# Kernel optimization log

Hardware: AMD Instinct MI355X
Metric: run time of the kernel (lower is better)

## Reference

```python
import jax, jax.numpy as jnp
import numpy as np

N = 100_000      # total nodes in batched graph
NE = 800_000     # total edges
G = 1_000        # number of graphs in batch
V_DIM = 128      # node feat dim (== H_DIM, required by GRUCell usage)
E_DIM = 64       # edge feat dim
H_DIM = 128      # hidden dim
K_HEAD = 4       # multi-scale interaction heads


def _leaky(x):
    return jnp.where(x >= 0, x, 0.1 * x)


def _gru_cell(x, h, Wih, Whh, bih, bhh):
    # torch nn.GRUCell math; Wih/Whh stored as [in, 3*h] with (r,z,n) chunk order
    gi = x @ Wih + bih
    gh = h @ Whh + bhh
    ir, iz, inn = jnp.split(gi, 3, axis=-1)
    hr, hz, hn = jnp.split(gh, 3, axis=-1)
    r = jax.nn.sigmoid(ir + hr)
    z = jax.nn.sigmoid(iz + hz)
    n = jnp.tanh(inn + r * hn)
    return (1.0 - z) * n + z * h


def setup_inputs() -> dict:
    key = jax.random.key(0)
    ks = iter(jax.random.split(key, 48))
    def rn(shape, scale=0.05):
        return (jax.random.normal(next(ks), shape) * scale).astype(jnp.float32)
    inp = {}
    inp["v"] = rn((N, V_DIM), 1.0)
    inp["e"] = rn((NE, E_DIM), 1.0)
    inp["s"] = rn((G, V_DIM), 1.0)
    inp["edge_src"] = jax.random.randint(next(ks), (NE,), 0, N)
    inp["edge_dst"] = jax.random.randint(next(ks), (NE,), 0, N)
    inp["node_graph"] = jnp.repeat(jnp.arange(G), N // G)  # sorted segment ids
    # top-level linears (stored [in, out])
    inp["A_w"] = rn((V_DIM, H_DIM)); inp["A_b"] = rn((H_DIM,))
    inp["mA_w"] = rn((K_HEAD, V_DIM, H_DIM)); inp["mA_b"] = rn((K_HEAD, H_DIM))
    inp["mB_w"] = rn((K_HEAD, V_DIM, H_DIM)); inp["mB_b"] = rn((K_HEAD, H_DIM))
    inp["mC_w"] = rn((K_HEAD, H_DIM)); inp["mC_b"] = rn((K_HEAD,))
    inp["mD_w"] = rn((K_HEAD, V_DIM, H_DIM)); inp["mD_b"] = rn((K_HEAD, H_DIM))
    inp["B_w"] = rn((H_DIM * K_HEAD, H_DIM)); inp["B_b"] = rn((H_DIM,))
    inp["C_w"] = rn((V_DIM, H_DIM)); inp["C_b"] = rn((H_DIM,))
    inp["K_w"] = rn((E_DIM, H_DIM)); inp["K_b"] = rn((H_DIM,))
    inp["E_w"] = rn((H_DIM + V_DIM, H_DIM)); inp["E_b"] = rn((H_DIM,))
    for pfx in ("gm", "gs"):
        inp[pfx + "_A_w"] = rn((H_DIM, H_DIM)); inp[pfx + "_A_b"] = rn((H_DIM,))
        inp[pfx + "_B_w"] = rn((H_DIM, H_DIM)); inp[pfx + "_B_b"] = rn((H_DIM,))
        inp[pfx + "_Wih"] = rn((H_DIM, 3 * H_DIM)); inp[pfx + "_Whh"] = rn((H_DIM, 3 * H_DIM))
        inp[pfx + "_bih"] = rn((3 * H_DIM,)); inp[pfx + "_bhh"] = rn((3 * H_DIM,))
    return inp


def reference(v, e, s, edge_src, edge_dst, node_graph,
              A_w, A_b, mA_w, mA_b, mB_w, mB_b, mC_w, mC_b, mD_w, mD_b,
              B_w, B_b, C_w, C_b, K_w, K_b, E_w, E_b,
              gm_A_w, gm_A_b, gm_B_w, gm_B_b, gm_Wih, gm_Whh, gm_bih, gm_bhh,
              gs_A_w, gs_A_b, gs_B_w, gs_B_b, gs_Wih, gs_Whh, gs_bih, gs_bhh):
    # super -> super
    s2s = jnp.tanh(s @ A_w + A_b)                                       # [G,H]
    # multi-head node->super attention pooling (Multi_scale_interaction)
    d_node = jnp.tanh(jnp.einsum('nv,kvh->knh', v, mA_w) + mA_b[:, None, :])     # [K,N,H]
    d_super = jnp.tanh(jnp.einsum('gv,kvh->kgh', s, mB_w) + mB_b[:, None, :])    # [K,G,H]
    a = jnp.einsum('knh,kh->nk', d_node * d_super[:, node_graph, :], mC_w) + mC_b[None, :]  # [N,K]
    a_max = jax.ops.segment_max(a, node_graph, num_segments=G, indices_are_sorted=True)
    a_exp = jnp.exp(a - a_max[node_graph])
    denom = jax.ops.segment_sum(a_exp, node_graph, num_segments=G, indices_are_sorted=True)
    attn = a_exp / denom[node_graph]                                    # per-graph softmax, [N,K]
    d_v = jnp.einsum('nv,kvh->nkh', v, mD_w) + mD_b[None, :, :]         # [N,K,H]
    pooled = jax.ops.segment_sum(d_v * attn[:, :, None], node_graph, num_segments=G,
                                 indices_are_sorted=True)               # [G,K,H]
    m2s = jnp.tanh(pooled.reshape(G, K_HEAD * H_DIM) @ B_w + B_b)       # [G,H]
    # super -> node broadcast
    s2m = jnp.tanh(s @ C_w + C_b)[node_graph]                           # [N,H]
    # edge-wise message: leaky_relu(K(e) * v_src) summed into destination node
    ve = _leaky((e @ K_w + K_b) * v[edge_src])                          # [E,H]
    sve = jax.ops.segment_sum(ve, edge_dst, num_segments=N)             # [N,H]
    m2m = _leaky(jnp.concatenate([sve, v], axis=1) @ E_w + E_b)         # [N,H]
    # adaptive GRU gate: node update
    z_m = jax.nn.sigmoid(m2m @ gm_A_w + gm_A_b + s2m @ gm_B_w + gm_B_b)
    h_m = z_m * s2m + (1.0 - z_m) * m2m
    update_v = _gru_cell(v, h_m, gm_Wih, gm_Whh, gm_bih, gm_bhh)
    # adaptive GRU gate: supernode update
    z_s = jax.nn.sigmoid(s2s @ gs_A_w + gs_A_b + m2s @ gs_B_w + gs_B_b)
    h_s = z_s * m2s + (1.0 - z_s) * s2s
    update_s = _gru_cell(s, h_s, gs_Wih, gs_Whh, gs_bih, gs_bhh)
    return (update_v, update_s)
```

## Files before the change

kernel.cpp:

```cpp
#include <hip/hip_runtime.h>

#define NN   100000
#define NEDG 800000
#define NG   1000
#define HD   128
#define EDIM 64

#define NB3 (NEDG / 64)
#define NB2 ((NN + 63) / 64)
#define NB6 ((NN + 63) / 64)
#define NB4 (NN / 32)

typedef unsigned short u16;
typedef __bf16 bf16x8 __attribute__((ext_vector_type(8)));
typedef float f32x4 __attribute__((ext_vector_type(4)));
typedef u16 u16x8 __attribute__((ext_vector_type(8)));
typedef unsigned u32x4 __attribute__((ext_vector_type(4)));

#define MFMA16(a, b, c) __builtin_amdgcn_mfma_f32_16x16x32_bf16(a, b, c, 0, 0, 0)

#define WS_E    0
#define WS_GA   4096
#define WS_WIH  6144
#define WS_WHH  12288
#define WS_MA0  18432
#define WS_KW   26624
#define WS_LANES 27648

#define BF(base, NTT, ks, nt, lane) \
    (*(const bf16x8*)(wsw + (size_t)((base) + (((ks) * (NTT) + (nt)) * 64 + (lane))) * 8))

__device__ __forceinline__ float sigmoidf_(float x) { return 1.0f / (1.0f + __expf(-x)); }
__device__ __forceinline__ float tanhf_(float x) {
    float ax = fabsf(x);
    float e  = __expf(-2.0f * ax);
    float t  = (1.0f - e) / (1.0f + e);
    return copysignf(t, x);
}
__device__ __forceinline__ float leaky_(float x) { return x >= 0.f ? x : 0.1f * x; }
__device__ __forceinline__ u16 f2bf(float x) {
    union { float f; unsigned u; } c; c.f = x;
    unsigned r = c.u + 0x7FFF + ((c.u >> 16) & 1);
    return (u16)(r >> 16);
}
__device__ __forceinline__ float bfbits2f(unsigned hw) {
    union { unsigned u; float f; } c; c.u = hw << 16; return c.f;
}
__device__ __forceinline__ unsigned pack2bf(float lo, float hi) {
    return (unsigned)f2bf(lo) | ((unsigned)f2bf(hi) << 16);
}
__device__ __forceinline__ bf16x8 mk8(const float* __restrict__ p) {
    float4 a = *(const float4*)p;
    float4 b = *(const float4*)(p + 4);
    union { u32x4 u; bf16x8 v; } c;
    c.u[0] = pack2bf(a.x, a.y);
    c.u[1] = pack2bf(a.z, a.w);
    c.u[2] = pack2bf(b.x, b.y);
    c.u[3] = pack2bf(b.z, b.w);
    return c.v;
}

__device__ __forceinline__ void stg4(u16* lds, int P, int r, int c0, float4 v4) {
    int byteoff = (c0 << 1) ^ ((r & 7) << 4);
    u16* p = lds + r * P + (byteoff >> 1);
    p[0] = f2bf(v4.x); p[1] = f2bf(v4.y); p[2] = f2bf(v4.z); p[3] = f2bf(v4.w);
}
__device__ __forceinline__ void stg1(u16* lds, int P, int r, int c, u16 val) {
    int byteoff = (c << 1) ^ ((r & 7) << 4);
    lds[r * P + (byteoff >> 1)] = val;
}
__device__ __forceinline__ bf16x8 ldA(const u16* lds, int P, int r, int ks, int hi) {
    int byteoff = (ks * 64 + (hi << 4)) ^ ((r & 7) << 4);
    return *(const bf16x8*)(lds + r * P + (byteoff >> 1));
}

__global__ __launch_bounds__(256) void wconv(
    const float* __restrict__ E_w, const float* __restrict__ gmA_w,
    const float* __restrict__ Wih, const float* __restrict__ Whh,
    const float* __restrict__ mA_w, const float* __restrict__ K_w,
    u16* __restrict__ dst)
{
    int t = blockIdx.x * 256 + threadIdx.x;
    if (t >= WS_LANES) return;
    const float* W; int N; int local;
    if (t < 4096)       { W = E_w;  N = 128; local = t; }
    else if (t < 6144)  { W = gmA_w; N = 128; local = t - 4096; }
    else if (t < 12288) { W = Wih;  N = 384; local = t - 6144; }
    else if (t < 18432) { W = Whh;  N = 384; local = t - 12288; }
    else if (t < 26624) { int k = (t - 18432) >> 11; W = mA_w + k * 128 * 128; N = 128; local = (t - 18432) & 2047; }
    else                { W = K_w;  N = 128; local = t - 26624; }
    int lane = local & 63;
    int fid  = local >> 6;
    int NT = N >> 4;
    int ks = fid / NT, nt = fid - ks * NT;
    int krow = ks * 32 + ((lane >> 4) << 3);
    int col  = nt * 16 + (lane & 15);
    u16* d = dst + (size_t)t * 8;
    #pragma unroll
    for (int j = 0; j < 8; j++) d[j] = f2bf(W[(size_t)(krow + j) * N + col]);
}

__global__ __launch_bounds__(256) void k_hist(const int* __restrict__ edst, int* __restrict__ cnt) {
    int i = blockIdx.x * 256 + threadIdx.x;
    if (i < NEDG) atomicAdd(&cnt[edst[i]], 1);
}

__global__ __launch_bounds__(256) void k_scan1(const int* __restrict__ cnt,
                                               int* __restrict__ excl, int* __restrict__ bsum) {
    __shared__ int sd[256];
    int t = threadIdx.x, b = blockIdx.x;
    int base = b * 1024 + t * 4;
    int v0 = (base + 0 < NN) ? cnt[base + 0] : 0;
    int v1 = (base + 1 < NN) ? cnt[base + 1] : 0;
    int v2 = (base + 2 < NN) ? cnt[base + 2] : 0;
    int v3 = (base + 3 < NN) ? cnt[base + 3] : 0;
    int s = v0 + v1 + v2 + v3;
    sd[t] = s;
    __syncthreads();
    for (int off = 1; off < 256; off <<= 1) {
        int x = (t >= off) ? sd[t - off] : 0;
        __syncthreads();
        sd[t] += x;
        __syncthreads();
    }
    int incl = sd[t];
    int ex = incl - s;
    if (base + 0 < NN) excl[base + 0] = ex;
    if (base + 1 < NN) excl[base + 1] = ex + v0;
    if (base + 2 < NN) excl[base + 2] = ex + v0 + v1;
    if (base + 3 < NN) excl[base + 3] = ex + v0 + v1 + v2;
    if (t == 255) bsum[b] = incl;
}

#define NSCB 98
__global__ void k_scan2(int* __restrict__ bsum) {
    if (threadIdx.x == 0 && blockIdx.x == 0) {
        int run = 0;
        for (int i = 0; i < NSCB; i++) { int t = bsum[i]; bsum[i] = run; run += t; }
    }
}

__global__ __launch_bounds__(256) void k_scan3(const int* __restrict__ excl,
                                               const int* __restrict__ bsum,
                                               int* __restrict__ start) {
    int i = blockIdx.x * 256 + threadIdx.x;
    if (i < NN) start[i] = excl[i] + bsum[i >> 10];
}

__global__ __launch_bounds__(256) void k_scatter(const int* __restrict__ edst,
                                                 int* __restrict__ start,
                                                 int* __restrict__ perm) {
    int i = blockIdx.x * 256 + threadIdx.x;
    if (i < NEDG) {
        int pos = atomicAdd(&start[edst[i]], 1);
        perm[pos] = i;
    }
}

__global__ __launch_bounds__(128) void k1_graph(
    const float* __restrict__ s,
    const float* __restrict__ A_w, const float* __restrict__ A_b,
    const float* __restrict__ mB_w, const float* __restrict__ mB_b,
    const float* __restrict__ mC_w,
    const float* __restrict__ C_w, const float* __restrict__ C_b,
    const float* __restrict__ gmB_w, const float* __restrict__ gmA_b, const float* __restrict__ gmB_b,
    float* __restrict__ s2s, float* __restrict__ wkg,
    float* __restrict__ s2m_tab, float* __restrict__ t2)
{
    __shared__ float sm[HD];
    __shared__ float sm2[HD];
    const int g = blockIdx.x, t = threadIdx.x;
    sm[t] = s[g * HD + t];
    __syncthreads();
    {
        float a = 0.f;
        #pragma unroll 8
        for (int i = 0; i < HD; i++) a = fmaf(sm[i], A_w[i * HD + t], a);
        s2s[g * HD + t] = tanhf_(a + A_b[t]);
    }
    for (int k = 0; k < 4; k++) {
        float a = 0.f;
        const float* W = mB_w + k * HD * HD;
        #pragma unroll 8
        for (int i = 0; i < HD; i++) a = fmaf(sm[i], W[i * HD + t], a);
        float d = tanhf_(a + mB_b[k * HD + t]);
        wkg[(k * NG + g) * HD + t] = d * mC_w[k * HD + t];
    }
    float s2m;
    {
        float a = 0.f;
        #pragma unroll 8
        for (int i = 0; i < HD; i++) a = fmaf(sm[i], C_w[i * HD + t], a);
        s2m = tanhf_(a + C_b[t]);
        s2m_tab[g * HD + t] = s2m;
    }
    sm2[t] = s2m;
    __syncthreads();
    {
        float a = 0.f;
        #pragma unroll 8
        for (int i = 0; i < HD; i++) a = fmaf(sm2[i], gmB_w[i * HD + t], a);
        t2[g * HD + t] = a + gmA_b[t] + gmB_b[t];
    }
}

__global__ __launch_bounds__(256) void k2_standalone(
    const float* __restrict__ v, const int* __restrict__ ngr,
    const u16* __restrict__ wsw,
    const float* __restrict__ mA_b, const float* __restrict__ mC_b,
    const float* __restrict__ wkg,
    float* __restrict__ aexp, float* __restrict__ denom)
{
    const int tid = threadIdx.x;
    const int lane = tid & 63, w = tid >> 6;
    const int l15 = lane & 15, hi = lane >> 4;
    const int n0 = blockIdx.x * 64 + w * 16;
    const int arow = min(n0 + l15, NN - 1);
    bf16x8 av[4];
    #pragma unroll
    for (int ks = 0; ks < 4; ks++)
        av[ks] = mk8(v + (size_t)arow * HD + ks * 32 + hi * 8);
    int gq[4], nodeq[4];
    #pragma unroll
    for (int q = 0; q < 4; q++) {
        int nd = n0 + hi * 4 + q;
        nodeq[q] = nd;
        gq[q] = ngr[min(nd, NN - 1)];
    }
    for (int k = 0; k < 4; k++) {
        float rs[4] = {0.f, 0.f, 0.f, 0.f};
        const float* bias = mA_b + k * HD;
        #pragma unroll
        for (int nt = 0; nt < 8; nt++) {
            f32x4 acc = {0.f, 0.f, 0.f, 0.f};
            #pragma unroll
            for (int ks = 0; ks < 4; ks++)
                acc = MFMA16(av[ks], BF(WS_MA0 + k * 2048, 8, ks, nt, lane), acc);
            int col = nt * 16 + l15;
            float bb = bias[col];
            #pragma unroll
            for (int q = 0; q < 4; q++)
                rs[q] += tanhf_(acc[q] + bb) * wkg[((size_t)k * NG + gq[q]) * HD + col];
        }
        #pragma unroll
        for (int q = 0; q < 4; q++) {
            float x = rs[q];
            x += __shfl_xor(x, 1); x += __shfl_xor(x, 2);
            x += __shfl_xor(x, 4); x += __shfl_xor(x, 8);
            if (l15 == 0 && nodeq[q] < NN) {
                float ev = __expf(x + mC_b[k]);
                aexp[(size_t)nodeq[q] * 4 + k] = ev;
                atomicAdd(&denom[gq[q] * 4 + k], ev);
            }
        }
    }
}

#define OPW 66
__global__ __launch_bounds__(256) void k3_merge(
    const float* __restrict__ e, const float* __restrict__ v,
    const int* __restrict__ esrc, const int* __restrict__ edst,
    const int* __restrict__ perm,
    const u16* __restrict__ wsw, const float* __restrict__ K_b,
    float* __restrict__ sve)
{
    __shared__ unsigned OUTP[64 * OPW];
    __shared__ int pid[64];
    __shared__ int dsta[64];
    const int tid = threadIdx.x;
    const int e0 = blockIdx.x * 64;
    if (tid < 64) {
        int p = perm[e0 + tid];
        pid[tid] = p;
        dsta[tid] = edst[p];
    }
    const int lane = tid & 63, w = tid >> 6;
    const int l15 = lane & 15, hi = lane >> 4;
    const int rbase = w * 16;
    const int myrow = perm[e0 + rbase + l15];
    bf16x8 ae[2];
    #pragma unroll
    for (int ks = 0; ks < 2; ks++)
        ae[ks] = mk8(e + (size_t)myrow * EDIM + ks * 32 + hi * 8);
    __syncthreads();
    int sq[4];
    #pragma unroll
    for (int q = 0; q < 4; q++) sq[q] = esrc[pid[rbase + hi * 4 + q]];
    u16* OU = (u16*)OUTP;
    #pragma unroll
    for (int nt = 0; nt < 8; nt++) {
        f32x4 acc = {0.f, 0.f, 0.f, 0.f};
        acc = MFMA16(ae[0], BF(WS_KW, 8, 0, nt, lane), acc);
        acc = MFMA16(ae[1], BF(WS_KW, 8, 1, nt, lane), acc);
        int col = nt * 16 + l15;
        float kb = K_b[col];
        #pragma unroll
        for (int q = 0; q < 4; q++) {
            float val = leaky_((acc[q] + kb) * v[(size_t)sq[q] * HD + col]);
            OU[(rbase + hi * 4 + q) * (OPW * 2) + col] = f2bf(val);
        }
    }
    __syncthreads();
    {
        const int cp = tid & 63;
        const int qr = tid >> 6;
        const int r0 = qr * 16;
        int dcur = dsta[r0];
        unsigned x = OUTP[r0 * OPW + cp];
        float a0 = bfbits2f(x & 0xffff), a1 = bfbits2f(x >> 16);
        #pragma unroll
        for (int i = 1; i < 16; i++) {
            int r = r0 + i;
            int d = dsta[r];
            unsigned y = OUTP[r * OPW + cp];
            float y0 = bfbits2f(y & 0xffff), y1 = bfbits2f(y >> 16);
            if (d == dcur) { a0 += y0; a1 += y1; }
            else {
                atomicAdd(&sve[(size_t)dcur * HD + cp * 2 + 0], a0);
                atomicAdd(&sve[(size_t)dcur * HD + cp * 2 + 1], a1);
                dcur = d; a0 = y0; a1 = y1;
            }
        }
        atomicAdd(&sve[(size_t)dcur * HD + cp * 2 + 0], a0);
        atomicAdd(&sve[(size_t)dcur * HD + cp * 2 + 1], a1);
    }
}

__global__ __launch_bounds__(256) void k3_edge_unsorted(
    const float* __restrict__ e, const float* __restrict__ v,
    const int* __restrict__ esrc, const int* __restrict__ edst,
    const u16* __restrict__ wsw, const float* __restrict__ K_b,
    float* __restrict__ sve)
{
    const int tid = threadIdx.x;
    const int e0 = blockIdx.x * 64;
    const int lane = tid & 63, w = tid >> 6;
    const int l15 = lane & 15, hi = lane >> 4;
    const int rbase = w * 16;
    const int myrow = e0 + rbase + l15;
    bf16x8 ae[2];
    #pragma unroll
    for (int ks = 0; ks < 2; ks++)
        ae[ks] = mk8(e + (size_t)myrow * EDIM + ks * 32 + hi * 8);
    int sq[4], dq[4];
    #pragma unroll
    for (int q = 0; q < 4; q++) {
        int ei = e0 + rbase + hi * 4 + q;
        sq[q] = esrc[ei]; dq[q] = edst[ei];
    }
    #pragma unroll
    for (int nt = 0; nt < 8; nt++) {
        f32x4 acc = {0.f, 0.f, 0.f, 0.f};
        acc = MFMA16(ae[0], BF(WS_KW, 8, 0, nt, lane), acc);
        acc = MFMA16(ae[1], BF(WS_KW, 8, 1, nt, lane), acc);
        int col = nt * 16 + l15;
        float kb = K_b[col];
        #pragma unroll
        for (int q = 0; q < 4; q++) {
            float val = leaky_((acc[q] + kb) * v[(size_t)sq[q] * HD + col]);
            atomicAdd(&sve[(size_t)dq[q] * HD + col], val);
        }
    }
}

__device__ __forceinline__ void k4_body(
    int bid, int tid,
    const float* __restrict__ v, const int* __restrict__ ngr,
    const float* __restrict__ aexp, const float* __restrict__ denom,
    float* __restrict__ vbar)
{
    const int d = tid & 127;
    const int hf = tid >> 7;
    const int n0 = bid * 32 + hf * 16;
    int gcur = -1;
    float a0 = 0.f, a1 = 0.f, a2 = 0.f, a3 = 0.f;
    float4 rd = make_float4(0.f, 0.f, 0.f, 0.f);
    for (int nd = 0; nd < 16; nd++) {
        int n = n0 + nd;
        int g = ngr[n];
        if (g != gcur) {
            if (gcur >= 0) {
                atomicAdd(&vbar[(gcur * 4 + 0) * HD + d], a0);
                atomicAdd(&vbar[(gcur * 4 + 1) * HD + d], a1);
                atomicAdd(&vbar[(gcur * 4 + 2) * HD + d], a2);
                atomicAdd(&vbar[(gcur * 4 + 3) * HD + d], a3);
                a0 = a1 = a2 = a3 = 0.f;
            }
            float4 dn = *(const float4*)&denom[g * 4];
            rd = make_float4(1.f / dn.x, 1.f / dn.y, 1.f / dn.z, 1.f / dn.w);
            gcur = g;
        }
        float4 ae = *(const float4*)&aexp[n * 4];
        float vv = v[(size_t)n * HD + d];
        a0 = fmaf(ae.x * rd.x, vv, a0);
        a1 = fmaf(ae.y * rd.y, vv, a1);
        a2 = fmaf(ae.z * rd.z, vv, a2);
        a3 = fmaf(ae.w * rd.w, vv, a3);
    }
    atomicAdd(&vbar[(gcur * 4 + 0) * HD + d], a0);
    atomicAdd(&vbar[(gcur * 4 + 1) * HD + d], a1);
    atomicAdd(&vbar[(gcur * 4 + 2) * HD + d], a2);
    atomicAdd(&vbar[(gcur * 4 + 3) * HD + d], a3);
}

__device__ __forceinline__ void k6_body(
    int bid, int tid, u16* T,
    const float* __restrict__ v, const int* __restrict__ ngr,
    const float* __restrict__ sve, const u16* __restrict__ wsw,
    const float* __restrict__ E_b,
    const float* __restrict__ s2m_tab, const float* __restrict__ t2,
    const float* __restrict__ bih, const float* __restrict__ bhh,
    float* __restrict__ out_v)
{
    const int lane = tid & 63;
    const int l15 = lane & 15, hi = lane >> 4;
    const int n0 = bid * 64 + (tid >> 6) * 16;
    const int arow = min(n0 + l15, NN - 1);
    bf16x8 av[4], ax[4];
    #pragma unroll
    for (int ks = 0; ks < 4; ks++) {
        av[ks] = mk8(v   + (size_t)arow * HD + ks * 32 + hi * 8);
        ax[ks] = mk8(sve + (size_t)arow * HD + ks * 32 + hi * 8);
    }
    int gq[4], nodeq[4];
    #pragma unroll
    for (int q = 0; q < 4; q++) {
        int nd = n0 + hi * 4 + q;
        nodeq[q] = nd;
        gq[q] = ngr[min(nd, NN - 1)];
    }
    unsigned m2mp[8][2];
    #pragma unroll
    for (int nt = 0; nt < 8; nt++) {
        f32x4 acc = {0.f, 0.f, 0.f, 0.f};
        #pragma unroll
        for (int ks = 0; ks < 4; ks++) acc = MFMA16(ax[ks], BF(WS_E, 8, ks, nt, lane), acc);
        #pragma unroll
        for (int ks = 0; ks < 4; ks++) acc = MFMA16(av[ks], BF(WS_E, 8, 4 + ks, nt, lane), acc);
        float eb = E_b[nt * 16 + l15];
        float m0 = leaky_(acc[0] + eb), m1 = leaky_(acc[1] + eb);
        float m2 = leaky_(acc[2] + eb), m3 = leaky_(acc[3] + eb);
        m2mp[nt][0] = pack2bf(m0, m1);
        m2mp[nt][1] = pack2bf(m2, m3);
        int col = nt * 16 + l15;
        stg1(T, 128, hi * 4 + 0, col, (u16)(m2mp[nt][0] & 0xffff));
        stg1(T, 128, hi * 4 + 1, col, (u16)(m2mp[nt][0] >> 16));
        stg1(T, 128, hi * 4 + 2, col, (u16)(m2mp[nt][1] & 0xffff));
        stg1(T, 128, hi * 4 + 3, col, (u16)(m2mp[nt][1] >> 16));
    }
    bf16x8 am[4];
    #pragma unroll
    for (int ks = 0; ks < 4; ks++) am[ks] = ldA(T, 128, l15, ks, hi);
    unsigned hmp[8][2];
    #pragma unroll
    for (int nt = 0; nt < 8; nt++) {
        f32x4 acc = {0.f, 0.f, 0.f, 0.f};
        #pragma unroll
        for (int ks = 0; ks < 4; ks++) acc = MFMA16(am[ks], BF(WS_GA, 8, ks, nt, lane), acc);
        int col = nt * 16 + l15;
        float m2mq[4] = { bfbits2f(m2mp[nt][0] & 0xffff), bfbits2f(m2mp[nt][0] >> 16),
                          bfbits2f(m2mp[nt][1] & 0xffff), bfbits2f(m2mp[nt][1] >> 16) };
        float hm[4];
        #pragma unroll
        for (int q = 0; q < 4; q++) {
            int g = gq[q];
            float z = sigmoidf_(acc[q] + t2[(size_t)g * HD + col]);
            hm[q] = z * s2m_tab[(size_t)g * HD + col] + (1.f - z) * m2mq[q];
        }
        hmp[nt][0] = pack2bf(hm[0], hm[1]);
        hmp[nt][1] = pack2bf(hm[2], hm[3]);
        stg1(T, 128, hi * 4 + 0, col, (u16)(hmp[nt][0] & 0xffff));
        stg1(T, 128, hi * 4 + 1, col, (u16)(hmp[nt][0] >> 16));
        stg1(T, 128, hi * 4 + 2, col, (u16)(hmp[nt][1] & 0xffff));
        stg1(T, 128, hi * 4 + 3, col, (u16)(hmp[nt][1] >> 16));
    }
    bf16x8 ah[4];
    #pragma unroll
    for (int ks = 0; ks < 4; ks++) ah[ks] = ldA(T, 128, l15, ks, hi);
    #pragma unroll
    for (int nt = 0; nt < 8; nt++) {
        f32x4 air = {0.f,0.f,0.f,0.f}, aiz = {0.f,0.f,0.f,0.f}, ain = {0.f,0.f,0.f,0.f};
        f32x4 ahr = {0.f,0.f,0.f,0.f}, ahz = {0.f,0.f,0.f,0.f}, ahn = {0.f,0.f,0.f,0.f};
        #pragma unroll
        for (int ks = 0; ks < 4; ks++) {
            air = MFMA16(av[ks], BF(WS_WIH, 24, ks, nt,      lane), air);
            ahr = MFMA16(ah[ks], BF(WS_WHH, 24, ks, nt,      lane), ahr);
            aiz = MFMA16(av[ks], BF(WS_WIH, 24, ks, nt + 8,  lane), aiz);
            ahz = MFMA16(ah[ks], BF(WS_WHH, 24, ks, nt + 8,  lane), ahz);
            ain = MFMA16(av[ks], BF(WS_WIH, 24, ks, nt + 16, lane), ain);
            ahn = MFMA16(ah[ks], BF(WS_WHH, 24, ks, nt + 16, lane), ahn);
        }
        int col = nt * 16 + l15;
        float br  = bih[col] + bhh[col];
        float bz  = bih[HD + col] + bhh[HD + col];
        float bi3 = bih[2 * HD + col];
        float bh3 = bhh[2 * HD + col];
        float hmq[4] = { bfbits2f(hmp[nt][0] & 0xffff), bfbits2f(hmp[nt][0] >> 16),
                         bfbits2f(hmp[nt][1] & 0xffff), bfbits2f(hmp[nt][1] >> 16) };
        #pragma unroll
        for (int q = 0; q < 4; q++) {
            float r   = sigmoidf_(air[q] + ahr[q] + br);
            float z   = sigmoidf_(aiz[q] + ahz[q] + bz);
            float nnv = tanhf_(ain[q] + bi3 + r * (ahn[q] + bh3));
            if (nodeq[q] < NN)
                out_v[(size_t)nodeq[q] * HD + col] = (1.f - z) * nnv + z * hmq[q];
        }
    }
}

__global__ __launch_bounds__(256) void mega2(
    const float* __restrict__ v, const int* __restrict__ ngr,
    const float* __restrict__ sve, const u16* __restrict__ wsw,
    const float* __restrict__ E_b,
    const float* __restrict__ s2m_tab, const float* __restrict__ t2,
    const float* __restrict__ bih, const float* __restrict__ bhh,
    const float* __restrict__ aexp, const float* __restrict__ denom,
    float* __restrict__ out_v, float* __restrict__ vbar)
{
    __shared__ u16 TT[4][16 * 128];
    const int bid = blockIdx.x, tid = threadIdx.x;
    if (bid < NB6) {
        k6_body(bid, tid, TT[tid >> 6], v, ngr, sve, wsw, E_b, s2m_tab, t2, bih, bhh, out_v);
    } else {
        k4_body(bid - NB6, tid, v, ngr, aexp, denom, vbar);
    }
}

__global__ __launch_bounds__(128) void k5_super(
    const float* __restrict__ s, const float* __restrict__ vbar,
    const float* __restrict__ mD_w, const float* __restrict__ mD_b,
    const float* __restrict__ B_w, const float* __restrict__ B_b,
    const float* __restrict__ s2s,
    const float* __restrict__ gsA_w, const float* __restrict__ gsA_b,
    const float* __restrict__ gsB_w, const float* __restrict__ gsB_b,
    const float* __restrict__ gsWih, const float* __restrict__ gsWhh,
    const float* __restrict__ gsbih, const float* __restrict__ gsbhh,
    float* __restrict__ out_s)
{
    __shared__ float vb[4 * HD];
    __shared__ float p[4 * HD];
    __shared__ float m2s_l[HD];
    __shared__ float s2s_l[HD];
    __shared__ float hs_l[HD];
    __shared__ float srow[HD];
    const int g = blockIdx.x, t = threadIdx.x;
    #pragma unroll
    for (int l = 0; l < 4; l++) vb[t + HD * l] = vbar[(size_t)g * 4 * HD + t + HD * l];
    srow[t]  = s[g * HD + t];
    s2s_l[t] = s2s[g * HD + t];
    __syncthreads();
    for (int k = 0; k < 4; k++) {
        float a = 0.f;
        const float* W = mD_w + k * HD * HD;
        #pragma unroll 8
        for (int i = 0; i < HD; i++) a = fmaf(vb[k * HD + i], W[i * HD + t], a);
        p[k * HD + t] = a + mD_b[k * HD + t];
    }
    __syncthreads();
    float m2s;
    {
        float a = 0.f;
        #pragma unroll 8
        for (int j = 0; j < 4 * HD; j++) a = fmaf(p[j], B_w[j * HD + t], a);
        m2s = tanhf_(a + B_b[t]);
        m2s_l[t] = m2s;
    }
    __syncthreads();
    float hs;
    {
        float za = 0.f, zb = 0.f;
        #pragma unroll 8
        for (int i = 0; i < HD; i++) {
            za = fmaf(s2s_l[i], gsA_w[i * HD + t], za);
            zb = fmaf(m2s_l[i], gsB_w[i * HD + t], zb);
        }
        float z = sigmoidf_(za + gsA_b[t] + zb + gsB_b[t]);
        hs = z * m2s + (1.f - z) * s2s_l[t];
        hs_l[t] = hs;
    }
    __syncthreads();
    float gi0 = 0.f, gh0 = 0.f, gi1 = 0.f, gh1 = 0.f, gi2 = 0.f, gh2 = 0.f;
    #pragma unroll 4
    for (int i = 0; i < HD; i++) {
        float sv = srow[i], hv = hs_l[i];
        gi0 = fmaf(sv, gsWih[i * 384 + t], gi0);
        gh0 = fmaf(hv, gsWhh[i * 384 + t], gh0);
        gi1 = fmaf(sv, gsWih[i * 384 + 128 + t], gi1);
        gh1 = fmaf(hv, gsWhh[i * 384 + 128 + t], gh1);
        gi2 = fmaf(sv, gsWih[i * 384 + 256 + t], gi2);
        gh2 = fmaf(hv, gsWhh[i * 384 + 256 + t], gh2);
    }
    float r  = sigmoidf_(gi0 + gsbih[t] + gh0 + gsbhh[t]);
    float z2 = sigmoidf_(gi1 + gsbih[128 + t] + gh1 + gsbhh[128 + t]);
    float nn = tanhf_(gi2 + gsbih[256 + t] + r * (gh2 + gsbhh[256 + t]));
    out_s[g * HD + t] = (1.f - z2) * nn + z2 * hs;
}

extern "C" void kernel_launch(void* const* d_in, const int* in_sizes, int n_in,
                              void* d_out, int out_size, void* d_ws, size_t ws_size,
                              hipStream_t stream)
{
    const float* v    = (const float*)d_in[0];
    const float* e    = (const float*)d_in[1];
    const float* s    = (const float*)d_in[2];
    const int*   esrc = (const int*)d_in[3];
    const int*   edst = (const int*)d_in[4];
    const int*   ngr  = (const int*)d_in[5];
    const float* A_w  = (const float*)d_in[6];
    const float* A_b  = (const float*)d_in[7];
    const float* mA_w = (const float*)d_in[8];
    const float* mA_b = (const float*)d_in[9];
    const float* mB_w = (const float*)d_in[10];
    const float* mB_b = (const float*)d_in[11];
    const float* mC_w = (const float*)d_in[12];
    const float* mC_b = (const float*)d_in[13];
    const float* mD_w = (const float*)d_in[14];
    const float* mD_b = (const float*)d_in[15];
    const float* B_w  = (const float*)d_in[16];
    const float* B_b  = (const float*)d_in[17];
    const float* C_w  = (const float*)d_in[18];
    const float* C_b  = (const float*)d_in[19];
    const float* K_w  = (const float*)d_in[20];
    const float* K_b  = (const float*)d_in[21];
    const float* E_w  = (const float*)d_in[22];
    const float* E_b  = (const float*)d_in[23];
    const float* gmA_w = (const float*)d_in[24];
    const float* gmA_b = (const float*)d_in[25];
    const float* gmB_w = (const float*)d_in[26];
    const float* gmB_b = (const float*)d_in[27];
    const float* gmWih = (const float*)d_in[28];
    const float* gmWhh = (const float*)d_in[29];
    const float* gmbih = (const float*)d_in[30];
    const float* gmbhh = (const float*)d_in[31];
    const float* gsA_w = (const float*)d_in[32];
    const float* gsA_b = (const float*)d_in[33];
    const float* gsB_w = (const float*)d_in[34];
    const float* gsB_b = (const float*)d_in[35];
    const float* gsWih = (const float*)d_in[36];
    const float* gsWhh = (const float*)d_in[37];
    const float* gsbih = (const float*)d_in[38];
    const float* gsbhh = (const float*)d_in[39];

    float* ws      = (float*)d_ws;
    float* sve     = ws;
    float* aexp    = sve + 12800000;
    float* denom   = aexp + 400000;
    float* wkg     = denom + 4000;
    float* s2s     = wkg + 512000;
    float* s2m_tab = s2s + 128000;
    float* t2      = s2m_tab + 128000;
    float* vbar    = t2 + 128000;
    u16*   wswz    = (u16*)(vbar + 512000);
    int*   isc     = (int*)(wswz + 221184);
    int*   cnt     = isc;
    int*   excl    = cnt + 100000;
    int*   bsum    = excl + 100000;
    int*   startp  = bsum + 128;
    int*   perm    = startp + 100000;
    const size_t NEED_SORT = ((size_t)(perm + 800000 - (int*)d_ws)) * 4;
    const bool do_sort = ws_size >= NEED_SORT;

    hipMemsetAsync(sve, 0, (size_t)12800000 * 4, stream);
    hipMemsetAsync(denom, 0, (size_t)4000 * 4, stream);
    hipMemsetAsync(vbar, 0, (size_t)512000 * 4, stream);

    float* out_v = (float*)d_out;
    float* out_s = out_v + (size_t)NN * HD;

    wconv<<<(WS_LANES + 255) / 256, 256, 0, stream>>>(E_w, gmA_w, gmWih, gmWhh, mA_w, K_w, wswz);
    k1_graph<<<NG, 128, 0, stream>>>(s, A_w, A_b, mB_w, mB_b, mC_w, C_w, C_b,
                                     gmB_w, gmA_b, gmB_b, s2s, wkg, s2m_tab, t2);
    if (do_sort) {
        hipMemsetAsync(cnt, 0, (size_t)100000 * 4, stream);
        k_hist<<<(NEDG + 255) / 256, 256, 0, stream>>>(edst, cnt);
        k_scan1<<<NSCB, 256, 0, stream>>>(cnt, excl, bsum);
        k_scan2<<<1, 64, 0, stream>>>(bsum);
        k_scan3<<<(NN + 255) / 256, 256, 0, stream>>>(excl, bsum, startp);
        k_scatter<<<(NEDG + 255) / 256, 256, 0, stream>>>(edst, startp, perm);
    }
    k2_standalone<<<NB2, 256, 0, stream>>>(v, ngr, wswz, mA_b, mC_b, wkg, aexp, denom);
    if (do_sort) {
        k3_merge<<<NB3, 256, 0, stream>>>(e, v, esrc, edst, perm, wswz, K_b, sve);
    } else {
        k3_edge_unsorted<<<NEDG / 64, 256, 0, stream>>>(e, v, esrc, edst, wswz, K_b, sve);
    }
    mega2<<<NB6 + NB4, 256, 0, stream>>>(v, ngr, sve, wswz, E_b, s2m_tab, t2,
                                         gmbih, gmbhh, aexp, denom, out_v, vbar);
    k5_super<<<NG, 128, 0, stream>>>(s, vbar, mD_w, mD_b, B_w, B_b, s2s,
                                     gsA_w, gsA_b, gsB_w, gsB_b,
                                     gsWih, gsWhh, gsbih, gsbhh, out_s);
}
```

Before: 710.9 us.

## Fuse setup kernels and memsets into combined launches, fold scan3 into scatter

Merges the weight conversion, per-graph kernel and all zero-fills (sve, cnt, vbar, denom) into one block-partitioned launch. It then co-launches the edge histogram with the attention-logit kernel. It also removes the separate start-offset kernel: the scatter now computes `excl+bsum` inline and ranks edges by decrementing the counts. The goal is to cut launch and memset overhead and the serialization gaps between small kernels. In exchange, grids become heterogeneous, and cnt is zeroed and histogrammed even on the unsorted path.

Result: faster. 679.7 us (median of 2 runs) (-4.4%).

```diff
diff --git a/kernel.cpp b/kernel.cpp
--- a/kernel.cpp
+++ b/kernel.cpp
@@ -10,6 +10,12 @@
 #define NB2 ((NN + 63) / 64)
 #define NB6 ((NN + 63) / 64)
 #define NB4 (NN / 32)
+#define W0B 108
+#define MH_HIST 3125
+#define Z_F4 3200000
+#define Z_TOT 3300000
+#define ZB ((Z_TOT + 255) / 256)
+#define M0_GRID (W0B + NG + ZB)
 
 typedef unsigned short u16;
 typedef __bf16 bf16x8 __attribute__((ext_vector_type(8)));
@@ -60,11 +66,6 @@
     return c.v;
 }
 
-__device__ __forceinline__ void stg4(u16* lds, int P, int r, int c0, float4 v4) {
-    int byteoff = (c0 << 1) ^ ((r & 7) << 4);
-    u16* p = lds + r * P + (byteoff >> 1);
-    p[0] = f2bf(v4.x); p[1] = f2bf(v4.y); p[2] = f2bf(v4.z); p[3] = f2bf(v4.w);
-}
 __device__ __forceinline__ void stg1(u16* lds, int P, int r, int c, u16 val) {
     int byteoff = (c << 1) ^ ((r & 7) << 4);
     lds[r * P + (byteoff >> 1)] = val;
@@ -74,14 +75,13 @@
     return *(const bf16x8*)(lds + r * P + (byteoff >> 1));
 }
 
-__global__ __launch_bounds__(256) void wconv(
+__device__ __forceinline__ void wconv_body(
+    int t,
     const float* __restrict__ E_w, const float* __restrict__ gmA_w,
     const float* __restrict__ Wih, const float* __restrict__ Whh,
     const float* __restrict__ mA_w, const float* __restrict__ K_w,
     u16* __restrict__ dst)
 {
-    int t = blockIdx.x * 256 + threadIdx.x;
-    if (t >= WS_LANES) return;
     const float* W; int N; int local;
     if (t < 4096)       { W = E_w;  N = 128; local = t; }
     else if (t < 6144)  { W = gmA_w; N = 128; local = t - 4096; }
@@ -100,9 +100,158 @@
     for (int j = 0; j < 8; j++) d[j] = f2bf(W[(size_t)(krow + j) * N + col]);
 }
 
-__global__ __launch_bounds__(256) void k_hist(const int* __restrict__ edst, int* __restrict__ cnt) {
-    int i = blockIdx.x * 256 + threadIdx.x;
-    if (i < NEDG) atomicAdd(&cnt[edst[i]], 1);
+__device__ __forceinline__ void k1_body(
+    int g, int t,
+    const float* __restrict__ s,
+    const float* __restrict__ A_w, const float* __restrict__ A_b,
+    const float* __restrict__ mB_w, const float* __restrict__ mB_b,
+    const float* __restrict__ mC_w,
+    const float* __restrict__ C_w, const float* __restrict__ C_b,
+    const float* __restrict__ gmB_w, const float* __restrict__ gmA_b, const float* __restrict__ gmB_b,
+    float* __restrict__ s2s, float* __restrict__ wkg,
+    float* __restrict__ s2m_tab, float* __restrict__ t2,
+    float* __restrict__ vbar, float* __restrict__ denom)
+{
+    __shared__ float sm[HD];
+    __shared__ float sm2[HD];
+    if (t < HD) sm[t] = s[g * HD + t];
+    else {
+        int i = t - 128;
+        #pragma unroll
+        for (int j = 0; j < 4; j++) vbar[(size_t)g * 512 + i + 128 * j] = 0.f;
+        if (i < 4) denom[g * 4 + i] = 0.f;
+    }
+    __syncthreads();
+    float s2m = 0.f;
+    if (t < HD) {
+        {
+            float a = 0.f;
+            #pragma unroll 8
+            for (int i = 0; i < HD; i++) a = fmaf(sm[i], A_w[i * HD + t], a);
+            s2s[g * HD + t] = tanhf_(a + A_b[t]);
+        }
+        for (int k = 0; k < 4; k++) {
+            float a = 0.f;
+            const float* W = mB_w + k * HD * HD;
+            #pragma unroll 8
+            for (int i = 0; i < HD; i++) a = fmaf(sm[i], W[i * HD + t], a);
+            float d = tanhf_(a + mB_b[k * HD + t]);
+            wkg[(k * NG + g) * HD + t] = d * mC_w[k * HD + t];
+        }
+        {
+            float a = 0.f;
+            #pragma unroll 8
+            for (int i = 0; i < HD; i++) a = fmaf(sm[i], C_w[i * HD + t], a);
+            s2m = tanhf_(a + C_b[t]);
+            s2m_tab[g * HD + t] = s2m;
+            sm2[t] = s2m;
+        }
+    }
+    __syncthreads();
+    if (t < HD) {
+        float a = 0.f;
+        #pragma unroll 8
+        for (int i = 0; i < HD; i++) a = fmaf(sm2[i], gmB_w[i * HD + t], a);
+        t2[g * HD + t] = a + gmA_b[t] + gmB_b[t];
+    }
+}
+
+__global__ __launch_bounds__(256) void mega0(
+    const float* __restrict__ E_w, const float* __restrict__ gmA_w,
+    const float* __restrict__ Wih, const float* __restrict__ Whh,
+    const float* __restrict__ mA_w, const float* __restrict__ K_w,
+    u16* __restrict__ wswz,
+    const float* __restrict__ s,
+    const float* __restrict__ A_w, const float* __restrict__ A_b,
+    const float* __restrict__ mB_w, const float* __restrict__ mB_b,
+    const float* __restrict__ mC_w,
+    const float* __restrict__ C_w, const float* __restrict__ C_b,
+    const float* __restrict__ gmB_w, const float* __restrict__ gmA_b, const float* __restrict__ gmB_b,
+    float* __restrict__ s2s, float* __restrict__ wkg,
+    float* __restrict__ s2m_tab, float* __restrict__ t2,
+    float* __restrict__ vbar, float* __restrict__ denom,
+    float* __restrict__ sve, int* __restrict__ cnt)
+{
+    const int bid = blockIdx.x, tid = threadIdx.x;
+    if (bid < W0B) {
+        wconv_body(bid * 256 + tid, E_w, gmA_w, Wih, Whh, mA_w, K_w, wswz);
+    } else if (bid < W0B + NG) {
+        k1_body(bid - W0B, tid, s, A_w, A_b, mB_w, mB_b, mC_w, C_w, C_b,
+                gmB_w, gmA_b, gmB_b, s2s, wkg, s2m_tab, t2, vbar, denom);
+    } else {
+        long idx = (long)(bid - W0B - NG) * 256 + tid;
+        if (idx < Z_F4) ((float4*)sve)[idx] = make_float4(0.f, 0.f, 0.f, 0.f);
+        else if (idx < Z_TOT) cnt[idx - Z_F4] = 0;
+    }
+}
+
+__device__ __forceinline__ void k2_body(
+    int bid, int tid,
+    const float* __restrict__ v, const int* __restrict__ ngr,
+    const u16* __restrict__ wsw,
+    const float* __restrict__ mA_b, const float* __restrict__ mC_b,
+    const float* __restrict__ wkg,
+    float* __restrict__ aexp, float* __restrict__ denom)
+{
+    const int lane = tid & 63, w = tid >> 6;
+    const int l15 = lane & 15, hi = lane >> 4;
+    const int n0 = bid * 64 + w * 16;
+    const int arow = min(n0 + l15, NN - 1);
+    bf16x8 av[4];
+    #pragma unroll
+    for (int ks = 0; ks < 4; ks++)
+        av[ks] = mk8(v + (size_t)arow * HD + ks * 32 + hi * 8);
+    int gq[4], nodeq[4];
+    #pragma unroll
+    for (int q = 0; q < 4; q++) {
+        int nd = n0 + hi * 4 + q;
+        nodeq[q] = nd;
+        gq[q] = ngr[min(nd, NN - 1)];
+    }
+    for (int k = 0; k < 4; k++) {
+        float rs[4] = {0.f, 0.f, 0.f, 0.f};
+        const float* bias = mA_b + k * HD;
+        #pragma unroll
+        for (int nt = 0; nt < 8; nt++) {
+            f32x4 acc = {0.f, 0.f, 0.f, 0.f};
+            #pragma unroll
+            for (int ks = 0; ks < 4; ks++)
+                acc = MFMA16(av[ks], BF(WS_MA0 + k * 2048, 8, ks, nt, lane), acc);
+            int col = nt * 16 + l15;
+            float bb = bias[col];
+            #pragma unroll
+            for (int q = 0; q < 4; q++)
+                rs[q] += tanhf_(acc[q] + bb) * wkg[((size_t)k * NG + gq[q]) * HD + col];
+        }
+        #pragma unroll
+        for (int q = 0; q < 4; q++) {
+            float x = rs[q];
+            x += __shfl_xor(x, 1); x += __shfl_xor(x, 2);
+            x += __shfl_xor(x, 4); x += __shfl_xor(x, 8);
+            if (l15 == 0 && nodeq[q] < NN) {
+                float ev = __expf(x + mC_b[k]);
+                aexp[(size_t)nodeq[q] * 4 + k] = ev;
+                atomicAdd(&denom[gq[q] * 4 + k], ev);
+            }
+        }
+    }
+}
+
+__global__ __launch_bounds__(256) void megaH(
+    const int* __restrict__ edst, int* __restrict__ cnt,
+    const float* __restrict__ v, const int* __restrict__ ngr,
+    const u16* __restrict__ wsw,
+    const float* __restrict__ mA_b, const float* __restrict__ mC_b,
+    const float* __restrict__ wkg,
+    float* __restrict__ aexp, float* __restrict__ denom)
+{
+    const int bid = blockIdx.x, tid = threadIdx.x;
+    if (bid < MH_HIST) {
+        int i = bid * 256 + tid;
+        if (i < NEDG) atomicAdd(&cnt[edst[i]], 1);
+    } else {
+        k2_body(bid - MH_HIST, tid, v, ngr, wsw, mA_b, mC_b, wkg, aexp, denom);
+    }
 }
 
 __global__ __launch_bounds__(256) void k_scan1(const int* __restrict__ cnt,
@@ -140,119 +289,16 @@
     }
 }
 
-__global__ __launch_bounds__(256) void k_scan3(const int* __restrict__ excl,
-                                               const int* __restrict__ bsum,
-                                               int* __restrict__ start) {
-    int i = blockIdx.x * 256 + threadIdx.x;
-    if (i < NN) start[i] = excl[i] + bsum[i >> 10];
-}
-
-__global__ __launch_bounds__(256) void k_scatter(const int* __restrict__ edst,
-                                                 int* __restrict__ start,
-                                                 int* __restrict__ perm) {
+__global__ __launch_bounds__(256) void k_scatter_fused(
+    const int* __restrict__ edst,
+    const int* __restrict__ excl, const int* __restrict__ bsum,
+    int* __restrict__ cnt, int* __restrict__ perm)
+{
     int i = blockIdx.x * 256 + threadIdx.x;
     if (i < NEDG) {
-        int pos = atomicAdd(&start[edst[i]], 1);
-        perm[pos] = i;
-    }
-}
-
-__global__ __launch_bounds__(128) void k1_graph(
-    const float* __restrict__ s,
-    const float* __restrict__ A_w, const float* __restrict__ A_b,
-    const float* __restrict__ mB_w, const float* __restrict__ mB_b,
-    const float* __restrict__ mC_w,
-    const float* __restrict__ C_w, const float* __restrict__ C_b,
-    const float* __restrict__ gmB_w, const float* __restrict__ gmA_b, const float* __restrict__ gmB_b,
-    float* __restrict__ s2s, float* __restrict__ wkg,
-    float* __restrict__ s2m_tab, float* __restrict__ t2)
-{
-    __shared__ float sm[HD];
-    __shared__ float sm2[HD];
-    const int g = blockIdx.x, t = threadIdx.x;
-    sm[t] = s[g * HD + t];
-    __syncthreads();
-    {
-        float a = 0.f;
-        #pragma unroll 8
-        for (int i = 0; i < HD; i++) a = fmaf(sm[i], A_w[i * HD + t], a);
-        s2s[g * HD + t] = tanhf_(a + A_b[t]);
-    }
-    for (int k = 0; k < 4; k++) {
-        float a = 0.f;
-        const float* W = mB_w + k * HD * HD;
-        #pragma unroll 8
-        for (int i = 0; i < HD; i++) a = fmaf(sm[i], W[i * HD + t], a);
-        float d = tanhf_(a + mB_b[k * HD + t]);
-        wkg[(k * NG + g) * HD + t] = d * mC_w[k * HD + t];
-    }
-    float s2m;
-    {
-        float a = 0.f;
-        #pragma unroll 8
-        for (int i = 0; i < HD; i++) a = fmaf(sm[i], C_w[i * HD + t], a);
-        s2m = tanhf_(a + C_b[t]);
-        s2m_tab[g * HD + t] = s2m;
-    }
-    sm2[t] = s2m;
-    __syncthreads();
-    {
-        float a = 0.f;
-        #pragma unroll 8
-        for (int i = 0; i < HD; i++) a = fmaf(sm2[i], gmB_w[i * HD + t], a);
-        t2[g * HD + t] = a + gmA_b[t] + gmB_b[t];
-    }
-}
-
-__global__ __launch_bounds__(256) void k2_standalone(
-    const float* __restrict__ v, const int* __restrict__ ngr,
-    const u16* __restrict__ wsw,
-    const float* __restrict__ mA_b, const float* __restrict__ mC_b,
-    const float* __restrict__ wkg,
-    float* __restrict__ aexp, float* __restrict__ denom)
-{
-    const int tid = threadIdx.x;
-    const int lane = tid & 63, w = tid >> 6;
-    const int l15 = lane & 15, hi = lane >> 4;
-    const int n0 = blockIdx.x * 64 + w * 16;
-    const int arow = min(n0 + l15, NN - 1);
-    bf16x8 av[4];
-    #pragma unroll
-    for (int ks = 0; ks < 4; ks++)
-        av[ks] = mk8(v + (size_t)arow * HD + ks * 32 + hi * 8);
-    int gq[4], nodeq[4];
-    #pragma unroll
-    for (int q = 0; q < 4; q++) {
-        int nd = n0 + hi * 4 + q;
-        nodeq[q] = nd;
-        gq[q] = ngr[min(nd, NN - 1)];
-    }
-    for (int k = 0; k < 4; k++) {
-        float rs[4] = {0.f, 0.f, 0.f, 0.f};
-        const float* bias = mA_b + k * HD;
-        #pragma unroll
-        for (int nt = 0; nt < 8; nt++) {
-            f32x4 acc = {0.f, 0.f, 0.f, 0.f};
-            #pragma unroll
-            for (int ks = 0; ks < 4; ks++)
-                acc = MFMA16(av[ks], BF(WS_MA0 + k * 2048, 8, ks, nt, lane), acc);
-            int col = nt * 16 + l15;
-            float bb = bias[col];
-            #pragma unroll
-            for (int q = 0; q < 4; q++)
-                rs[q] += tanhf_(acc[q] + bb) * wkg[((size_t)k * NG + gq[q]) * HD + col];
-        }
-        #pragma unroll
-        for (int q = 0; q < 4; q++) {
-            float x = rs[q];
-            x += __shfl_xor(x, 1); x += __shfl_xor(x, 2);
-            x += __shfl_xor(x, 4); x += __shfl_xor(x, 8);
-            if (l15 == 0 && nodeq[q] < NN) {
-                float ev = __expf(x + mC_b[k]);
-                aexp[(size_t)nodeq[q] * 4 + k] = ev;
-                atomicAdd(&denom[gq[q] * 4 + k], ev);
-            }
-        }
+        int d = edst[i];
+        int rank = atomicSub(&cnt[d], 1) - 1;
+        perm[excl[d] + bsum[d >> 10] + rank] = i;
     }
 }
 
@@ -660,26 +706,19 @@
     const size_t NEED_SORT = ((size_t)(perm + 800000 - (int*)d_ws)) * 4;
     const bool do_sort = ws_size >= NEED_SORT;
 
-    hipMemsetAsync(sve, 0, (size_t)12800000 * 4, stream);
-    hipMemsetAsync(denom, 0, (size_t)4000 * 4, stream);
-    hipMemsetAsync(vbar, 0, (size_t)512000 * 4, stream);
-
     float* out_v = (float*)d_out;
     float* out_s = out_v + (size_t)NN * HD;
 
-    wconv<<<(WS_LANES + 255) / 256, 256, 0, stream>>>(E_w, gmA_w, gmWih, gmWhh, mA_w, K_w, wswz);
-    k1_graph<<<NG, 128, 0, stream>>>(s, A_w, A_b, mB_w, mB_b, mC_w, C_w, C_b,
-                                     gmB_w, gmA_b, gmB_b, s2s, wkg, s2m_tab, t2);
+    mega0<<<M0_GRID, 256, 0, stream>>>(E_w, gmA_w, gmWih, gmWhh, mA_w, K_w, wswz,
+                                       s, A_w, A_b, mB_w, mB_b, mC_w, C_w, C_b,
+                                       gmB_w, gmA_b, gmB_b, s2s, wkg, s2m_tab, t2,
+                                       vbar, denom, sve, cnt);
+    megaH<<<MH_HIST + NB2, 256, 0, stream>>>(edst, cnt, v, ngr, wswz, mA_b, mC_b,
+                                             wkg, aexp, denom);
     if (do_sort) {
-        hipMemsetAsync(cnt, 0, (size_t)100000 * 4, stream);
-        k_hist<<<(NEDG + 255) / 256, 256, 0, stream>>>(edst, cnt);
         k_scan1<<<NSCB, 256, 0, stream>>>(cnt, excl, bsum);
         k_scan2<<<1, 64, 0, stream>>>(bsum);
-        k_scan3<<<(NN + 255) / 256, 256, 0, stream>>>(excl, bsum, startp);
-        k_scatter<<<(NEDG + 255) / 256, 256, 0, stream>>>(edst, startp, perm);
-    }
-    k2_standalone<<<NB2, 256, 0, stream>>>(v, ngr, wswz, mA_b, mC_b, wkg, aexp, denom);
-    if (do_sort) {
+        k_scatter_fused<<<(NEDG + 255) / 256, 256, 0, stream>>>(edst, excl, bsum, cnt, perm);
         k3_merge<<<NB3, 256, 0, stream>>>(e, v, esrc, edst, perm, wswz, K_b, sve);
     } else {
         k3_edge_unsorted<<<NEDG / 64, 256, 0, stream>>>(e, v, esrc, edst, wswz, K_b, sve);
```
